# Kernel tuning notes

Hardware: AMD Instinct MI355X
Metric: run time of the kernel (lower is better)

## Reference

```python
import jax, jax.numpy as jnp
import numpy as np

H = 2048
EPS = 1e-12

def setup_inputs() -> dict:
    key = jax.random.key(0)
    ks = jax.random.split(key, 12)
    B, S = 2, 4096
    scale = 1.0 / np.sqrt(H)
    inp = {
        "hidden_states": jax.random.normal(ks[0], (B, S, H), dtype=jnp.float32),
        "token_type_ids": jax.random.randint(ks[1], (B, S), 0, 2, dtype=jnp.int32),
        "ln_gamma": jnp.ones((H,), jnp.float32),
        "ln_beta": jnp.zeros((H,), jnp.float32),
        "tw1": jax.random.uniform(ks[2], (H, H), jnp.float32, -scale, scale),
        "tb1": jnp.zeros((H,), jnp.float32),
        "tw2": jax.random.uniform(ks[3], (H, H), jnp.float32, -scale, scale),
        "tb2": jnp.zeros((H,), jnp.float32),
        "iw1": jax.random.uniform(ks[4], (H, H), jnp.float32, -scale, scale),
        "ib1": jnp.zeros((H,), jnp.float32),
        "iw2": jax.random.uniform(ks[5], (H, H), jnp.float32, -scale, scale),
        "ib2": jnp.zeros((H,), jnp.float32),
    }
    return inp

def _layernorm(x, g, b):
    mu = jnp.mean(x, axis=-1, keepdims=True)
    var = jnp.mean(jnp.square(x - mu), axis=-1, keepdims=True)
    return (x - mu) * jax.lax.rsqrt(var + EPS) * g + b

def _mlp(x, w1, b1, w2, b2):
    # Linear -> exact GELU -> Linear (torch nn.GELU default is erf-based)
    h = jax.nn.gelu(jnp.einsum('bsh,hk->bsk', x, w1) + b1, approximate=False)
    return jnp.einsum('bsk,kh->bsh', h, w2) + b2

def reference(hidden_states, token_type_ids, ln_gamma, ln_beta,
              tw1, tb1, tw2, tb2, iw1, ib1, iw2, ib2):
    xn = _layernorm(hidden_states, ln_gamma, ln_beta)
    text_mask = (token_type_ids == 0)[..., None]   # [B,S,1]
    image_mask = (token_type_ids == 1)[..., None]
    text_out = _mlp(xn, tw1, tb1, tw2, tb2) * text_mask
    image_out = _mlp(xn, iw1, ib1, iw2, ib2) * image_mask
    # dropout is identity in inference / p=0
    return hidden_states + text_out + image_out
```

## Files before the change

kernel.cpp:

```cpp
#include <hip/hip_runtime.h>
#include <hip/hip_bf16.h>


#define H_DIM 2048
#define FULLROWS 8192
#define TAILROWS 512

typedef __attribute__((ext_vector_type(8))) short s16x8;
typedef __attribute__((ext_vector_type(4))) float f32x4;
typedef __attribute__((ext_vector_type(4))) int   i32x4;

typedef __attribute__((address_space(1))) const unsigned int gu32;
typedef __attribute__((address_space(3))) unsigned int lu32;
typedef __attribute__((address_space(3))) short lds_s;

__device__ __forceinline__ void load_lds16(const void* g, void* l) {
  __builtin_amdgcn_global_load_lds((gu32*)g, (lu32*)l, 16, 0, 0);
}

__device__ __forceinline__ s16x8 asbf(i32x4 v) {
  union { i32x4 i; s16x8 s; } u; u.i = v; return u.s;
}

__global__ __launch_bounds__(256) void partition_kernel(
    const int* __restrict__ tt, int T, int* __restrict__ ctrl,
    int* __restrict__ pos, int* __restrict__ rowid) {
  __shared__ int psum[256];
  const int tid = threadIdx.x;
  const int npt = T >> 8;
  const int base = tid * npt;
  int cnt = 0;
  for (int i = 0; i < npt; ++i) cnt += (tt[base + i] == 0);
  psum[tid] = cnt;
  __syncthreads();
  for (int off = 1; off < 256; off <<= 1) {
    int v = psum[tid];
    int add = (tid >= off) ? psum[tid - off] : 0;
    __syncthreads();
    psum[tid] = v + add;
    __syncthreads();
  }
  const int Mt = psum[255];
  const int Mt_pad = (Mt + 255) & ~255;
  int tpos = psum[tid] - cnt;
  int ipos = base - tpos;
  for (int i = 0; i < npt; ++i) {
    const int tok = base + i;
    int p;
    if (tt[tok] == 0) p = tpos++;
    else              p = Mt_pad + ipos++;
    pos[tok] = p;
    rowid[p] = tok;
  }
  const int Mi = T - Mt;
  const int Mi_pad = (Mi + 255) & ~255;
  for (int g = Mt + tid; g < Mt_pad; g += 256) rowid[g] = -1;
  for (int g = Mt_pad + Mi + tid; g < Mt_pad + Mi_pad; g += 256) rowid[g] = -1;
  for (int g = Mt_pad + Mi_pad + tid; g < FULLROWS + TAILROWS; g += 256)
    rowid[g] = -1;
  if (tid == 0) {
    ctrl[0] = Mt; ctrl[1] = Mt_pad; ctrl[2] = Mi; ctrl[3] = Mi_pad;
    ctrl[4] = Mt_pad + Mi_pad;
  }
}

__global__ __launch_bounds__(256) void transpose_to_bf16(
    const float* __restrict__ W, __hip_bfloat16* __restrict__ WT) {
  __shared__ float tile[32][33];
  const int bx = blockIdx.x, by = blockIdx.y;
  const int tid = threadIdx.x;
  const int r = tid >> 3, c4 = (tid & 7) * 4;
  const float4 v = *(const float4*)(W + (size_t)(by * 32 + r) * H_DIM + bx * 32 + c4);
  tile[r][c4 + 0] = v.x; tile[r][c4 + 1] = v.y;
  tile[r][c4 + 2] = v.z; tile[r][c4 + 3] = v.w;
  __syncthreads();
  union { ushort u[4]; ushort4 v4; } pk;
#pragma unroll
  for (int j = 0; j < 4; ++j) {
    __hip_bfloat16 h = __float2bfloat16(tile[c4 + j][r]);
    pk.u[j] = *(const ushort*)&h;
  }
  *(ushort4*)(WT + (size_t)(bx * 32 + r) * H_DIM + by * 32 + c4) = pk.v4;
}

__global__ __launch_bounds__(256) void ln_scatter_kernel(
    const float* __restrict__ X, const float* __restrict__ gamma,
    const float* __restrict__ beta, const int* __restrict__ pos,
    __hip_bfloat16* __restrict__ XG) {
  const int t = blockIdx.x, tid = threadIdx.x;
  const float* row = X + (size_t)t * H_DIM;
  float x[8];
  {
    float4 v0 = *(const float4*)(row + tid * 8);
    float4 v1 = *(const float4*)(row + tid * 8 + 4);
    x[0] = v0.x; x[1] = v0.y; x[2] = v0.z; x[3] = v0.w;
    x[4] = v1.x; x[5] = v1.y; x[6] = v1.z; x[7] = v1.w;
  }
  float s = 0.f, q = 0.f;
#pragma unroll
  for (int j = 0; j < 8; ++j) { s += x[j]; q += x[j] * x[j]; }
#pragma unroll
  for (int off = 32; off > 0; off >>= 1) {
    s += __shfl_down(s, off);
    q += __shfl_down(q, off);
  }
  __shared__ float ls[4], lq[4];
  if ((tid & 63) == 0) { ls[tid >> 6] = s; lq[tid >> 6] = q; }
  __syncthreads();
  const float S = ls[0] + ls[1] + ls[2] + ls[3];
  const float Q = lq[0] + lq[1] + lq[2] + lq[3];
  const float mu = S * (1.0f / H_DIM);
  const float var = Q * (1.0f / H_DIM) - mu * mu;
  const float rstd = rsqrtf(var + 1e-12f);
  const int p = pos[t];
  float4 g0 = *(const float4*)(gamma + tid * 8);
  float4 g1 = *(const float4*)(gamma + tid * 8 + 4);
  float4 b0 = *(const float4*)(beta + tid * 8);
  float4 b1 = *(const float4*)(beta + tid * 8 + 4);
  float g[8] = {g0.x, g0.y, g0.z, g0.w, g1.x, g1.y, g1.z, g1.w};
  float b[8] = {b0.x, b0.y, b0.z, b0.w, b1.x, b1.y, b1.z, b1.w};
  union { ushort u[8]; int4 v; } pk;
#pragma unroll
  for (int j = 0; j < 8; ++j) {
    float y = (x[j] - mu) * rstd * g[j] + b[j];
    __hip_bfloat16 h = __float2bfloat16(y);
    pk.u[j] = *(const ushort*)&h;
  }
  *(int4*)(XG + (size_t)p * H_DIM + tid * 8) = pk.v;
}

#define DSRD(dst, addr, OFF) \
  asm volatile("ds_read_b128 %0, %1 offset:" OFF : "=v"(dst) : "v"(addr))
#define PBAR asm volatile("s_barrier" ::: "memory")
#define SB0  __builtin_amdgcn_sched_barrier(0)
#define LGKM0 do { \
  asm volatile("s_waitcnt lgkmcnt(0)" ::: "memory"); SB0; } while (0)
#define VM0 asm volatile("s_waitcnt vmcnt(0)" ::: "memory")

__device__ __forceinline__ float gelu_exact(float z) {
  return 0.5f * z * (1.0f + erff(z * 0.70710678118654752f));
}

template <int EPI>
__global__ __launch_bounds__(512, 2) void gemmk(
    const __hip_bfloat16* __restrict__ A,
    const __hip_bfloat16* __restrict__ WTt, const __hip_bfloat16* __restrict__ WTi,
    const float* __restrict__ bt, const float* __restrict__ bi,
    const int* __restrict__ ctrl, const int* __restrict__ rowid,
    __hip_bfloat16* __restrict__ Hout,
    const float* __restrict__ resid, float* __restrict__ Out,
    float* __restrict__ pp) {
  constexpr int K = H_DIM;
  const int Mt_pad = ctrl[1];

  __shared__ __align__(16) char smem[131072];
  const unsigned sBase = (unsigned)(uintptr_t)(lds_s*)smem;

  const int tid = threadIdx.x;
  const int w = tid >> 6, l = tid & 63;
  const int bid = blockIdx.x;

  const int srow8 = l >> 3;
  const int sg = (l & 7) ^ srow8;
  const int r16 = l & 15;
  const int r4base = (l >> 4) * 4;
  const int hl = (l & 15) >> 1;
  const int gr = (((l & 1) << 2) | (l >> 4)) ^ hl;

  if (bid < 256) {
    constexpr int NT = K / 64;
    const int m0 = (bid >> 3) * 256;
    const int n0 = (bid & 7) * 256;
    const bool is_text = (m0 < Mt_pad);
    const short* Ag = (const short*)A;
    const short* Bg = (const short*)(is_text ? WTt : WTi);
    const float* bias = is_text ? bt : bi;

    const int wm = w >> 2, wn = w & 3;
    const int scol8 = sg * 8;

    auto stageA = [&](int bI, int h, int kk) {
#pragma unroll
      for (int c = 0; c < 2; ++c) {
        const short* src = Ag + (size_t)(m0 + h * 128 + c * 64 + w * 8 + srow8) * K + kk + scol8;
        load_lds16(src, smem + bI * 32768 + h * 16384 + (c * 4096 + w * 512) * 2);
      }
    };
    auto stageB = [&](int bI, int h, int kk) {
#pragma unroll
      for (int c = 0; c < 2; ++c) {
        const short* src = Bg + (size_t)(n0 + h * 128 + c * 64 + w * 8 + srow8) * K + kk + scol8;
        load_lds16(src, smem + 65536 + bI * 32768 + h * 16384 + (c * 4096 + w * 512) * 2);
      }
    };

    int off2[2];
#pragma unroll
    for (int ks = 0; ks < 2; ++ks)
      off2[ks] = r16 * 64 + (((ks * 4 + (l >> 4)) ^ (l & 7)) * 8);

    unsigned ardA[2][2], ardB[2][2];
#pragma unroll
    for (int bI = 0; bI < 2; ++bI)
#pragma unroll
      for (int ks = 0; ks < 2; ++ks) {
        ardA[bI][ks] = sBase + bI * 32768u + (unsigned)(wm * 16384 + off2[ks] * 2);
        ardB[bI][ks] = sBase + 65536u + bI * 32768u +
                       (unsigned)((wn >> 1) * 16384 + ((wn & 1) * 4096 + off2[ks]) * 2);
      }

    i32x4 a[4][2], b[4][2];
    f32x4 acc[8][4];
    const f32x4 zero = {0.f, 0.f, 0.f, 0.f};
#pragma unroll
    for (int i = 0; i < 8; ++i)
#pragma unroll
      for (int j = 0; j < 4; ++j) acc[i][j] = zero;

    auto mfmaQ = [&](int fmBase, int fnBase) {
#pragma unroll
      for (int fm = 0; fm < 4; ++fm)
#pragma unroll
        for (int fn = 0; fn < 2; ++fn)
#pragma unroll
          for (int ks = 0; ks < 2; ++ks)
            acc[fmBase + fm][fnBase + fn] = __builtin_amdgcn_mfma_f32_16x16x32_bf16(
                asbf(a[fm][ks]), asbf(b[fnBase + fn][ks]),
                acc[fmBase + fm][fnBase + fn], 0, 0, 0);
    };

#define TILE(C) do {                                                          \
    DSRD(a[0][0], ardA[C][0], "0");     DSRD(a[0][1], ardA[C][1], "0");       \
    DSRD(a[1][0], ardA[C][0], "2048");  DSRD(a[1][1], ardA[C][1], "2048");    \
    DSRD(a[2][0], ardA[C][0], "4096");  DSRD(a[2][1], ardA[C][1], "4096");    \
    DSRD(a[3][0], ardA[C][0], "6144");  DSRD(a[3][1], ardA[C][1], "6144");    \
    DSRD(b[0][0], ardB[C][0], "0");     DSRD(b[0][1], ardB[C][1], "0");       \
    DSRD(b[1][0], ardB[C][0], "2048");  DSRD(b[1][1], ardB[C][1], "2048");    \
    stageA(C ^ 1, 0, _kA);                                                    \
    PBAR; LGKM0;                                                              \
    __builtin_amdgcn_s_setprio(1); mfmaQ(0, 0); __builtin_amdgcn_s_setprio(0);\
    SB0; PBAR;                                                                \
    DSRD(b[2][0], ardB[C][0], "4096");  DSRD(b[2][1], ardB[C][1], "4096");    \
    DSRD(b[3][0], ardB[C][0], "6144");  DSRD(b[3][1], ardB[C][1], "6144");    \
    stageA(C ^ 1, 1, _kA);                                                    \
    PBAR; LGKM0;                                                              \
    __builtin_amdgcn_s_setprio(1); mfmaQ(0, 2); __builtin_amdgcn_s_setprio(0);\
    SB0; PBAR;                                                                \
    DSRD(a[0][0], ardA[C][0], "8192");  DSRD(a[0][1], ardA[C][1], "8192");    \
    DSRD(a[1][0], ardA[C][0], "10240"); DSRD(a[1][1], ardA[C][1], "10240");   \
    DSRD(a[2][0], ardA[C][0], "12288"); DSRD(a[2][1], ardA[C][1], "12288");   \
    DSRD(a[3][0], ardA[C][0], "14336"); DSRD(a[3][1], ardA[C][1], "14336");   \
    stageB(C, 0, _kB);                                                        \
    PBAR; LGKM0;                                                              \
    __builtin_amdgcn_s_setprio(1); mfmaQ(4, 2); __builtin_amdgcn_s_setprio(0);\
    SB0; PBAR;                                                                \
    stageB(C, 1, _kB);                                                        \
    asm volatile("s_waitcnt vmcnt(4)" ::: "memory");                          \
    PBAR; SB0;                                                                \
    __builtin_amdgcn_s_setprio(1); mfmaQ(4, 0); __builtin_amdgcn_s_setprio(0);\
    SB0; PBAR;                                                                \
  } while (0)

    stageA(0, 0, 0); stageA(0, 1, 0);
    stageB(0, 0, 0); stageB(0, 1, 0);
    stageB(1, 0, 64); stageB(1, 1, 64);
    asm volatile("s_waitcnt vmcnt(4)" ::: "memory");
    PBAR;

    int _kA, _kB;
    for (int t = 0; t < NT; t += 2) {
      _kA = (t + 1 < NT ? t + 1 : NT - 1) * 64;
      _kB = (t + 2 < NT ? t + 2 : NT - 1) * 64;
      TILE(0);
      _kA = (t + 2 < NT ? t + 2 : NT - 1) * 64;
      _kB = (t + 3 < NT ? t + 3 : NT - 1) * 64;
      TILE(1);
    }
#undef TILE
    asm volatile("s_waitcnt vmcnt(0) lgkmcnt(0)" ::: "memory");

    float bb[4];
#pragma unroll
    for (int fn = 0; fn < 4; ++fn) bb[fn] = bias[n0 + wn * 64 + fn * 16 + r16];
    if (EPI == 0) {
#pragma unroll
      for (int fm = 0; fm < 8; ++fm) {
        const int grow = m0 + wm * 128 + fm * 16 + r4base;
#pragma unroll
        for (int fn = 0; fn < 4; ++fn) {
          const int gcol = n0 + wn * 64 + fn * 16 + r16;
          f32x4 v = acc[fm][fn];
#pragma unroll
          for (int i = 0; i < 4; ++i)
            Hout[(size_t)(grow + i) * K + gcol] = __float2bfloat16(gelu_exact(v[i] + bb[fn]));
        }
      }
    } else {
#pragma unroll
      for (int fm = 0; fm < 8; ++fm) {
        const int grow = m0 + wm * 128 + fm * 16 + r4base;
        int rid[4];
#pragma unroll
        for (int i = 0; i < 4; ++i) rid[i] = rowid[grow + i];
#pragma unroll
        for (int fn = 0; fn < 4; ++fn) {
          const int gcol = n0 + wn * 64 + fn * 16 + r16;
          f32x4 v = acc[fm][fn];
#pragma unroll
          for (int i = 0; i < 4; ++i) {
            if (rid[i] >= 0) {
              const size_t o = (size_t)rid[i] * K + gcol;
              Out[o] = resid[o] + v[i] + bb[fn];
            }
          }
        }
      }
    }
  } else {
    const int tb = bid - 256;
    const int kp = tb & 3;
    const int n0 = ((tb >> 2) & 7) * 256;
    const int m0 = FULLROWS + (tb >> 5) * 128;
    const int kk0 = kp * 512;
    const bool is_text = (m0 < Mt_pad);
    const short* Ag = (const short*)A;
    const short* Bg = (const short*)(is_text ? WTt : WTi);

    const int wm = w >> 2, wn = w & 3;
    const int sRowAdj = sg >> 2;
    const int sKAdj = (sg & 3) * 8;

    auto stageA = [&](int bI, int kk) {
      const int mr = w * 8 + srow8;
      const short* src = Ag + (size_t)(m0 + mr * 2 + sRowAdj) * K + kk + sKAdj;
      load_lds16(src, smem + bI * 8192 + w * 1024);
    };
    auto stageB = [&](int bI, int c2, int kk) {
      const int mr = c2 * 64 + w * 8 + srow8;
      const short* src = Bg + (size_t)(n0 + mr * 2 + sRowAdj) * K + kk + sKAdj;
      load_lds16(src, smem + 16384 + bI * 16384 + c2 * 8192 + w * 1024);
    };

    unsigned ardA[2], ardB[2];
#pragma unroll
    for (int bI = 0; bI < 2; ++bI) {
      ardA[bI] = sBase + bI * 8192u + (unsigned)(wm * 4096 + hl * 128 + gr * 16);
      ardB[bI] = sBase + 16384u + bI * 16384u + (unsigned)(wn * 4096 + hl * 128 + gr * 16);
    }

    i32x4 a[4], b[4];
    f32x4 acc[4][4];
    const f32x4 zero = {0.f, 0.f, 0.f, 0.f};
#pragma unroll
    for (int i = 0; i < 4; ++i)
#pragma unroll
      for (int j = 0; j < 4; ++j) acc[i][j] = zero;

#define RD_TILE(C) do {                                                   \
    DSRD(a[0], ardA[C], "0");    DSRD(a[1], ardA[C], "1024");             \
    DSRD(a[2], ardA[C], "2048"); DSRD(a[3], ardA[C], "3072");             \
    DSRD(b[0], ardB[C], "0");    DSRD(b[1], ardB[C], "1024");             \
    DSRD(b[2], ardB[C], "2048"); DSRD(b[3], ardB[C], "3072");             \
  } while (0)

    stageA(0, kk0);
    stageB(0, 0, kk0); stageB(0, 1, kk0);
    VM0;
    PBAR;

    for (int i = 0; i < 16; ++i) {
      const int c = i & 1;
      const int kn = kk0 + (i + 1 < 16 ? i + 1 : 15) * 32;
      stageA(c ^ 1, kn);
      stageB(c ^ 1, 0, kn); stageB(c ^ 1, 1, kn);
      RD_TILE(c);
      LGKM0;
      __builtin_amdgcn_s_setprio(1);
#pragma unroll
      for (int f = 0; f < 4; ++f)
#pragma unroll
        for (int fn = 0; fn < 4; ++fn)
          acc[f][fn] = __builtin_amdgcn_mfma_f32_16x16x32_bf16(
              asbf(a[f]), asbf(b[fn]), acc[f][fn], 0, 0, 0);
      __builtin_amdgcn_s_setprio(0);
      SB0;
      VM0;
      PBAR;
    }
#undef RD_TILE
    asm volatile("s_waitcnt vmcnt(0) lgkmcnt(0)" ::: "memory");

    float* ppk = pp + (size_t)kp * TAILROWS * H_DIM;
    const int mrel = m0 - FULLROWS;
#pragma unroll
    for (int fm = 0; fm < 4; ++fm) {
      const int prow = mrel + wm * 64 + fm * 16 + r4base;
#pragma unroll
      for (int fn = 0; fn < 4; ++fn) {
        const int gcol = n0 + wn * 64 + fn * 16 + r16;
        f32x4 v = acc[fm][fn];
#pragma unroll
        for (int i = 0; i < 4; ++i)
          ppk[(size_t)(prow + i) * H_DIM + gcol] = v[i];
      }
    }
  }
}

template <int EPI>
__global__ __launch_bounds__(256) void combine_kernel(
    const float* __restrict__ pp, const float* __restrict__ bt,
    const float* __restrict__ bi, const int* __restrict__ ctrl,
    const int* __restrict__ rowid, __hip_bfloat16* __restrict__ Hout,
    const float* __restrict__ resid, float* __restrict__ Out) {
  const int u = blockIdx.x * 256 + threadIdx.x;
  const int r = u >> 9;
  const int c = (u & 511) * 4;
  const size_t off = (size_t)r * H_DIM + c;
  float4 s = *(const float4*)(pp + off);
  const float4 s1 = *(const float4*)(pp + (size_t)TAILROWS * H_DIM + off);
  const float4 s2 = *(const float4*)(pp + (size_t)2 * TAILROWS * H_DIM + off);
  const float4 s3 = *(const float4*)(pp + (size_t)3 * TAILROWS * H_DIM + off);
  s.x += s1.x + s2.x + s3.x; s.y += s1.y + s2.y + s3.y;
  s.z += s1.z + s2.z + s3.z; s.w += s1.w + s2.w + s3.w;
  const int grow = FULLROWS + r;
  const float* bias = (grow < ctrl[1]) ? bt : bi;
  const float4 bb = *(const float4*)(bias + c);
  if (EPI == 0) {
    union { ushort u4[4]; ushort4 v4; } pk;
    float z[4] = {s.x + bb.x, s.y + bb.y, s.z + bb.z, s.w + bb.w};
#pragma unroll
    for (int j = 0; j < 4; ++j) {
      __hip_bfloat16 h = __float2bfloat16(0.5f * z[j] * (1.0f + erff(z[j] * 0.70710678118654752f)));
      pk.u4[j] = *(const ushort*)&h;
    }
    *(ushort4*)(Hout + (size_t)grow * H_DIM + c) = pk.v4;
  } else {
    const int rid = rowid[grow];
    if (rid >= 0) {
      const size_t o = (size_t)rid * H_DIM + c;
      const float4 rv = *(const float4*)(resid + o);
      float4 ov;
      ov.x = rv.x + s.x + bb.x; ov.y = rv.y + s.y + bb.y;
      ov.z = rv.z + s.z + bb.z; ov.w = rv.w + s.w + bb.w;
      *(float4*)(Out + o) = ov;
    }
  }
}

extern "C" void kernel_launch(void* const* d_in, const int* in_sizes, int n_in,
                              void* d_out, int out_size, void* d_ws, size_t ws_size,
                              hipStream_t stream) {
  const float* hidden = (const float*)d_in[0];
  const int*   tt     = (const int*)d_in[1];
  const float* gamma  = (const float*)d_in[2];
  const float* beta   = (const float*)d_in[3];
  const float* tw1    = (const float*)d_in[4];
  const float* tb1    = (const float*)d_in[5];
  const float* tw2    = (const float*)d_in[6];
  const float* tb2    = (const float*)d_in[7];
  const float* iw1    = (const float*)d_in[8];
  const float* ib1    = (const float*)d_in[9];
  const float* iw2    = (const float*)d_in[10];
  const float* ib2    = (const float*)d_in[11];
  float* out = (float*)d_out;

  const int T = in_sizes[1];
  const int K = H_DIM;
  const int maxrows = FULLROWS + TAILROWS;

  char* ws = (char*)d_ws;
  int* ctrl  = (int*)(ws);
  int* pos   = (int*)(ws + 4096);
  int* rowid = (int*)(ws + 65536);
  const size_t WOFF = 131072;
  const size_t WSZ = (size_t)K * K * sizeof(__hip_bfloat16);
  __hip_bfloat16* tw1T = (__hip_bfloat16*)(ws + WOFF);
  __hip_bfloat16* tw2T = (__hip_bfloat16*)(ws + WOFF + WSZ);
  __hip_bfloat16* iw1T = (__hip_bfloat16*)(ws + WOFF + 2 * WSZ);
  __hip_bfloat16* iw2T = (__hip_bfloat16*)(ws + WOFF + 3 * WSZ);
  __hip_bfloat16* xg   = (__hip_bfloat16*)(ws + WOFF + 4 * WSZ);
  __hip_bfloat16* hb   = xg + (size_t)maxrows * K;
  float* pp = (float*)(hb + (size_t)maxrows * K);

  hipMemsetAsync(xg, 0, (size_t)maxrows * K * sizeof(__hip_bfloat16), stream);

  partition_kernel<<<1, 256, 0, stream>>>(tt, T, ctrl, pos, rowid);

  dim3 tg(K / 32, K / 32);
  transpose_to_bf16<<<tg, 256, 0, stream>>>(tw1, tw1T);
  transpose_to_bf16<<<tg, 256, 0, stream>>>(tw2, tw2T);
  transpose_to_bf16<<<tg, 256, 0, stream>>>(iw1, iw1T);
  transpose_to_bf16<<<tg, 256, 0, stream>>>(iw2, iw2T);

  ln_scatter_kernel<<<T, 256, 0, stream>>>(hidden, gamma, beta, pos, xg);

  gemmk<0><<<384, 512, 0, stream>>>(xg, tw1T, iw1T, tb1, ib1, ctrl, rowid,
                                    hb, nullptr, nullptr, pp);
  combine_kernel<0><<<1024, 256, 0, stream>>>(pp, tb1, ib1, ctrl, rowid,
                                              hb, nullptr, nullptr);
  gemmk<1><<<384, 512, 0, stream>>>(hb, tw2T, iw2T, tb2, ib2, ctrl, rowid,
                                    nullptr, hidden, out, pp);
  combine_kernel<1><<<1024, 256, 0, stream>>>(pp, tb2, ib2, ctrl, rowid,
                                              nullptr, hidden, out);
}
```

Baseline: 267.3 us.

## Raise tail split-K to 8, replace full memset with pad zeroing, reuse weight buffers

The tail GEMM blocks now split K eight ways instead of four, so the GEMM grid grows from 384 to 512 blocks and the combine kernel reduces eight partial slices. The full memset of the activation buffer is replaced by a small kernel that zeroes only the padding rows. The second-layer weight transposes move to after the first GEMM so two buffers can be reused. The aim is better CU occupancy on the tail and less memset traffic, at the cost of more partial-sum traffic and a serialised transpose between the GEMMs.

```diff
diff --git a/kernel.cpp b/kernel.cpp
--- a/kernel.cpp
+++ b/kernel.cpp
@@ -5,6 +5,7 @@
 #define H_DIM 2048
 #define FULLROWS 8192
 #define TAILROWS 512
+#define KSPLIT 8
 
 typedef __attribute__((ext_vector_type(8))) short s16x8;
 typedef __attribute__((ext_vector_type(4))) float f32x4;
@@ -62,6 +63,23 @@
     ctrl[0] = Mt; ctrl[1] = Mt_pad; ctrl[2] = Mi; ctrl[3] = Mi_pad;
     ctrl[4] = Mt_pad + Mi_pad;
   }
+}
+
+__global__ __launch_bounds__(256) void pad_zero_kernel(
+    const int* __restrict__ ctrl, __hip_bfloat16* __restrict__ XG) {
+  const int Mt = ctrl[0], Mt_pad = ctrl[1], Mi = ctrl[2];
+  const int n1 = Mt_pad - Mt;
+  const int start2 = Mt_pad + Mi;
+  const int b = blockIdx.x;
+  int row;
+  if (b < n1) row = Mt + b;
+  else {
+    const int b2 = b - n1;
+    if (start2 + b2 >= FULLROWS + TAILROWS) return;
+    row = start2 + b2;
+  }
+  const int4 z = {0, 0, 0, 0};
+  *(int4*)(XG + (size_t)row * H_DIM + threadIdx.x * 8) = z;
 }
 
 __global__ __launch_bounds__(256) void transpose_to_bf16(
@@ -318,10 +336,10 @@
     }
   } else {
     const int tb = bid - 256;
-    const int kp = tb & 3;
-    const int n0 = ((tb >> 2) & 7) * 256;
-    const int m0 = FULLROWS + (tb >> 5) * 128;
-    const int kk0 = kp * 512;
+    const int kp = tb & 7;
+    const int n0 = ((tb >> 3) & 7) * 256;
+    const int m0 = FULLROWS + (tb >> 6) * 128;
+    const int kk0 = kp * 256;
     const bool is_text = (m0 < Mt_pad);
     const short* Ag = (const short*)A;
     const short* Bg = (const short*)(is_text ? WTt : WTi);
@@ -368,9 +386,9 @@
     VM0;
     PBAR;
 
-    for (int i = 0; i < 16; ++i) {
+    for (int i = 0; i < 8; ++i) {
       const int c = i & 1;
-      const int kn = kk0 + (i + 1 < 16 ? i + 1 : 15) * 32;
+      const int kn = kk0 + (i + 1 < 8 ? i + 1 : 7) * 32;
       stageA(c ^ 1, kn);
       stageB(c ^ 1, 0, kn); stageB(c ^ 1, 1, kn);
       RD_TILE(c);
@@ -418,11 +436,11 @@
   const int c = (u & 511) * 4;
   const size_t off = (size_t)r * H_DIM + c;
   float4 s = *(const float4*)(pp + off);
-  const float4 s1 = *(const float4*)(pp + (size_t)TAILROWS * H_DIM + off);
-  const float4 s2 = *(const float4*)(pp + (size_t)2 * TAILROWS * H_DIM + off);
-  const float4 s3 = *(const float4*)(pp + (size_t)3 * TAILROWS * H_DIM + off);
-  s.x += s1.x + s2.x + s3.x; s.y += s1.y + s2.y + s3.y;
-  s.z += s1.z + s2.z + s3.z; s.w += s1.w + s2.w + s3.w;
+#pragma unroll
+  for (int k = 1; k < KSPLIT; ++k) {
+    const float4 sk = *(const float4*)(pp + (size_t)k * TAILROWS * H_DIM + off);
+    s.x += sk.x; s.y += sk.y; s.z += sk.z; s.w += sk.w;
+  }
   const int grow = FULLROWS + r;
   const float* bias = (grow < ctrl[1]) ? bt : bi;
   const float4 bb = *(const float4*)(bias + c);
@@ -475,31 +493,30 @@
   int* rowid = (int*)(ws + 65536);
   const size_t WOFF = 131072;
   const size_t WSZ = (size_t)K * K * sizeof(__hip_bfloat16);
-  __hip_bfloat16* tw1T = (__hip_bfloat16*)(ws + WOFF);
-  __hip_bfloat16* tw2T = (__hip_bfloat16*)(ws + WOFF + WSZ);
-  __hip_bfloat16* iw1T = (__hip_bfloat16*)(ws + WOFF + 2 * WSZ);
-  __hip_bfloat16* iw2T = (__hip_bfloat16*)(ws + WOFF + 3 * WSZ);
-  __hip_bfloat16* xg   = (__hip_bfloat16*)(ws + WOFF + 4 * WSZ);
+  __hip_bfloat16* wTs0 = (__hip_bfloat16*)(ws + WOFF);
+  __hip_bfloat16* wTs1 = (__hip_bfloat16*)(ws + WOFF + WSZ);
+  __hip_bfloat16* xg   = (__hip_bfloat16*)(ws + WOFF + 2 * WSZ);
   __hip_bfloat16* hb   = xg + (size_t)maxrows * K;
   float* pp = (float*)(hb + (size_t)maxrows * K);
 
-  hipMemsetAsync(xg, 0, (size_t)maxrows * K * sizeof(__hip_bfloat16), stream);
-
   partition_kernel<<<1, 256, 0, stream>>>(tt, T, ctrl, pos, rowid);
+  pad_zero_kernel<<<512, 256, 0, stream>>>(ctrl, xg);
 
   dim3 tg(K / 32, K / 32);
-  transpose_to_bf16<<<tg, 256, 0, stream>>>(tw1, tw1T);
-  transpose_to_bf16<<<tg, 256, 0, stream>>>(tw2, tw2T);
-  transpose_to_bf16<<<tg, 256, 0, stream>>>(iw1, iw1T);
-  transpose_to_bf16<<<tg, 256, 0, stream>>>(iw2, iw2T);
+  transpose_to_bf16<<<tg, 256, 0, stream>>>(tw1, wTs0);
+  transpose_to_bf16<<<tg, 256, 0, stream>>>(iw1, wTs1);
 
   ln_scatter_kernel<<<T, 256, 0, stream>>>(hidden, gamma, beta, pos, xg);
 
-  gemmk<0><<<384, 512, 0, stream>>>(xg, tw1T, iw1T, tb1, ib1, ctrl, rowid,
+  gemmk<0><<<512, 512, 0, stream>>>(xg, wTs0, wTs1, tb1, ib1, ctrl, rowid,
                                     hb, nullptr, nullptr, pp);
   combine_kernel<0><<<1024, 256, 0, stream>>>(pp, tb1, ib1, ctrl, rowid,
                                               hb, nullptr, nullptr);
-  gemmk<1><<<384, 512, 0, stream>>>(hb, tw2T, iw2T, tb2, ib2, ctrl, rowid,
+
+  transpose_to_bf16<<<tg, 256, 0, stream>>>(tw2, wTs0);
+  transpose_to_bf16<<<tg, 256, 0, stream>>>(iw2, wTs1);
+
+  gemmk<1><<<512, 512, 0, stream>>>(hb, wTs0, wTs1, tb2, ib2, ctrl, rowid,
                                     nullptr, hidden, out, pp);
   combine_kernel<1><<<1024, 256, 0, stream>>>(pp, tb2, ib2, ctrl, rowid,
                                               nullptr, hidden, out);
```

After: 274.6 us. 1.03x slower.
